# Performance work log

Hardware: AMD Instinct MI355X
Metric: run time of the kernel (lower is better)

The kernel has to match this reference:

```python
import jax, jax.numpy as jnp
import numpy as np

B, T, H = 32, 512, 1024

def setup_inputs() -> dict:
    key = jax.random.key(0)
    k1, k2, k3, k4, k5 = jax.random.split(key, 5)
    s = 1.0 / np.sqrt(H)  # torch LSTM init scale
    return {
        "x": jax.random.normal(k1, (B, T, H), dtype=jnp.float32),
        "w_ih": jax.random.uniform(k2, (4 * H, H), jnp.float32, -s, s),
        "w_hh": jax.random.uniform(k3, (4 * H, H), jnp.float32, -s, s),
        "b_ih": jax.random.uniform(k4, (4 * H,), jnp.float32, -s, s),
        "b_hh": jax.random.uniform(k5, (4 * H,), jnp.float32, -s, s),
    }

def reference(x, w_ih, w_hh, b_ih, b_hh):
    # Precompute input projections for all steps: [T, B, 4H]
    xg = jnp.einsum('bth,gh->tbg', x, w_ih) + b_ih + b_hh
    h0 = jnp.zeros((x.shape[0], H), x.dtype)
    c0 = jnp.zeros_like(h0)

    def step(carry, xg_t):
        h, c = carry
        gates = xg_t + h @ w_hh.T            # [B, 4H]
        i, f, g, o = jnp.split(gates, 4, axis=-1)  # torch order: i,f,g,o
        i = jax.nn.sigmoid(i)
        f = jax.nn.sigmoid(f)
        g = jnp.tanh(g)
        o = jax.nn.sigmoid(o)
        c = f * c + i * g
        h = o * jnp.tanh(c)
        return (h, c), None

    (h_n, _), _ = jax.lax.scan(step, (h0, c0), xg)
    return h_n  # [B, H] == h_n[0] in torch
```

## Files before the change

### kernel.cpp

```cpp
#include <hip/hip_runtime.h>
#include <cmath>

#define Tn 512
#define Bn 32
#define Hn 1024

typedef short bf16x8 __attribute__((ext_vector_type(8)));
typedef float f32x4 __attribute__((ext_vector_type(4)));

__device__ __forceinline__ unsigned short f2bf_rne(float f) {
    unsigned u = __float_as_uint(f);
    unsigned r = (u + 0x7fffu + ((u >> 16) & 1u)) >> 16;
    return (unsigned short)r;
}
__device__ __forceinline__ float bf2f(unsigned short h) {
    return __uint_as_float((unsigned)h << 16);
}
__device__ __forceinline__ bf16x8 cvt8(float4 a, float4 b) {
    union { unsigned u[4]; bf16x8 v; } o;
    o.u[0] = (unsigned)f2bf_rne(a.x) | ((unsigned)f2bf_rne(a.y) << 16);
    o.u[1] = (unsigned)f2bf_rne(a.z) | ((unsigned)f2bf_rne(a.w) << 16);
    o.u[2] = (unsigned)f2bf_rne(b.x) | ((unsigned)f2bf_rne(b.y) << 16);
    o.u[3] = (unsigned)f2bf_rne(b.z) | ((unsigned)f2bf_rne(b.w) << 16);
    return o.v;
}
__device__ __forceinline__ bf16x8 as_bf8(uint4 u) {
    union { uint4 q; bf16x8 v; } o; o.q = u; return o.v;
}

__device__ __forceinline__ void gstore_u32_sc(unsigned* p, unsigned v) {
    asm volatile("global_store_dword %0, %1, off sc0 sc1\n\t"
                 "s_waitcnt vmcnt(0)"
                 :: "v"(p), "v"(v) : "memory");
}
__device__ __forceinline__ uint4 gload_u4_sc(const unsigned* p) {
    uint4 r;
    asm volatile("global_load_dwordx4 %0, %1, off sc0 sc1\n\t"
                 "s_waitcnt vmcnt(0)"
                 : "=&v"(r) : "v"(p) : "memory");
    return r;
}
__device__ __forceinline__ void gload_h_sc(const unsigned short* b0,
                                           const unsigned short* b1,
                                           uint4* o0, uint4* o1) {
    asm volatile(
        "global_load_dwordx4 %0, %8, off sc0 sc1\n\t"
        "global_load_dwordx4 %1, %8, off offset:64 sc0 sc1\n\t"
        "global_load_dwordx4 %2, %8, off offset:128 sc0 sc1\n\t"
        "global_load_dwordx4 %3, %8, off offset:192 sc0 sc1\n\t"
        "global_load_dwordx4 %4, %9, off sc0 sc1\n\t"
        "global_load_dwordx4 %5, %9, off offset:64 sc0 sc1\n\t"
        "global_load_dwordx4 %6, %9, off offset:128 sc0 sc1\n\t"
        "global_load_dwordx4 %7, %9, off offset:192 sc0 sc1\n\t"
        "s_waitcnt vmcnt(0)"
        : "=&v"(o0[0]), "=&v"(o0[1]), "=&v"(o0[2]), "=&v"(o0[3]),
          "=&v"(o1[0]), "=&v"(o1[1]), "=&v"(o1[2]), "=&v"(o1[3])
        : "v"(b0), "v"(b1)
        : "memory");
}

__global__ void lstm_flags_init(unsigned* flags) { flags[threadIdx.x] = 0u; }

__global__ __launch_bounds__(512, 2) void lstm_persist_mfma(
    const float* __restrict__ x,
    const float* __restrict__ w_ih,
    const float* __restrict__ w_hh,
    const float* __restrict__ b_ih,
    const float* __restrict__ b_hh,
    unsigned short* __restrict__ hbuf,
    unsigned* __restrict__ flags,
    float* __restrict__ out)
{
    extern __shared__ char smem[];
    unsigned short* lds_w = (unsigned short*)smem;
    float* lds_r = (float*)(smem + 131584);
    float* lds_g = (float*)(smem + 131584 + 16384);

    const int tid = threadIdx.x;
    const int bj  = blockIdx.x;
    const int wv  = tid >> 6;
    const int ln  = tid & 63;
    const int l15 = ln & 15;
    const int qd  = ln >> 4;

    for (int i = 0; i < 16; ++i) {
        int slot = i * 512 + tid;
        int r    = slot >> 9;
        int f4   = slot & 511;
        int n    = (r >> 2) * Hn + bj * 4 + (r & 3);
        float4 v = (f4 < 256) ? ((const float4*)(w_ih + (size_t)n * Hn))[f4]
                              : ((const float4*)(w_hh + (size_t)n * Hn))[f4 - 256];
        unsigned short h0 = f2bf_rne(v.x), h1 = f2bf_rne(v.y);
        unsigned short h2 = f2bf_rne(v.z), h3 = f2bf_rne(v.w);
        unsigned short l0 = f2bf_rne(v.x - bf2f(h0)), l1 = f2bf_rne(v.y - bf2f(h1));
        unsigned short l2 = f2bf_rne(v.z - bf2f(h2)), l3 = f2bf_rne(v.w - bf2f(h3));
        uint2 ph, pl;
        ph.x = (unsigned)h0 | ((unsigned)h1 << 16);
        ph.y = (unsigned)h2 | ((unsigned)h3 << 16);
        pl.x = (unsigned)l0 | ((unsigned)l1 << 16);
        pl.y = (unsigned)l2 | ((unsigned)l3 << 16);
        *(uint2*)(lds_w + (size_t)r        * 2056 + f4 * 4) = ph;
        *(uint2*)(lds_w + (size_t)(r + 16) * 2056 + f4 * 4) = pl;
    }

    float bias0 = 0.f, bias1 = 0.f, bias2 = 0.f, bias3 = 0.f, creg = 0.f;
    if (tid < 128) {
        int col = bj * 4 + (tid & 3);
        bias0 = b_ih[col]          + b_hh[col];
        bias1 = b_ih[Hn + col]     + b_hh[Hn + col];
        bias2 = b_ih[2 * Hn + col] + b_hh[2 * Hn + col];
        bias3 = b_ih[3 * Hn + col] + b_hh[3 * Hn + col];
    }
    __syncthreads();

    const unsigned short* whi_base = lds_w + (size_t)l15 * 2056 + qd * 8;
    const unsigned short* wlo_base = lds_w + (size_t)(l15 + 16) * 2056 + qd * 8;
    const float* xr0 = x + (size_t)l15        * (Tn * Hn) + wv * 128 + qd * 8;
    const float* xr1 = x + (size_t)(16 + l15) * (Tn * Hn) + wv * 128 + qd * 8;
    const size_t hoff0 = (size_t)l15        * Hn + wv * 128 + qd * 8;
    const size_t hoff1 = (size_t)(16 + l15) * Hn + wv * 128 + qd * 8;

    float4 xa0[4], xb0[4], xa1[4], xb1[4];
    #pragma unroll
    for (int j = 0; j < 4; ++j) {
        xa0[j] = *(const float4*)(xr0 + j * 32);
        xb0[j] = *(const float4*)(xr0 + j * 32 + 4);
        xa1[j] = *(const float4*)(xr1 + j * 32);
        xb1[j] = *(const float4*)(xr1 + j * 32 + 4);
    }

    for (int t = 0; t < Tn; ++t) {
        f32x4 acc0 = {0.f, 0.f, 0.f, 0.f};
        f32x4 acc1 = {0.f, 0.f, 0.f, 0.f};

        float4 na0[4], nb0[4], na1[4], nb1[4];
        {
            const int tn = (t + 1 < Tn) ? (t + 1) : t;
            const float* p0 = xr0 + (size_t)tn * Hn;
            const float* p1 = xr1 + (size_t)tn * Hn;
            #pragma unroll
            for (int j = 0; j < 4; ++j) {
                na0[j] = *(const float4*)(p0 + j * 32);
                nb0[j] = *(const float4*)(p0 + j * 32 + 4);
                na1[j] = *(const float4*)(p1 + j * 32);
                nb1[j] = *(const float4*)(p1 + j * 32 + 4);
            }
        }

        #pragma unroll
        for (int j = 0; j < 4; ++j) {
            const int koff = wv * 128 + j * 32;
            bf16x8 ahi = *(const bf16x8*)(whi_base + koff);
            bf16x8 alo = *(const bf16x8*)(wlo_base + koff);
            bf16x8 bf0 = cvt8(xa0[j], xb0[j]);
            bf16x8 bf1 = cvt8(xa1[j], xb1[j]);
            acc0 = __builtin_amdgcn_mfma_f32_16x16x32_bf16(ahi, bf0, acc0, 0, 0, 0);
            acc0 = __builtin_amdgcn_mfma_f32_16x16x32_bf16(alo, bf0, acc0, 0, 0, 0);
            acc1 = __builtin_amdgcn_mfma_f32_16x16x32_bf16(ahi, bf1, acc1, 0, 0, 0);
            acc1 = __builtin_amdgcn_mfma_f32_16x16x32_bf16(alo, bf1, acc1, 0, 0, 0);
        }

        if (t > 0) {
            if (wv == 0) {
                const unsigned* fp = flags + ln * 4;
                for (;;) {
                    uint4 f = gload_u4_sc(fp);
                    unsigned mn = f.x < f.y ? f.x : f.y;
                    unsigned mo = f.z < f.w ? f.z : f.w;
                    mn = mn < mo ? mn : mo;
                    if (__all((int)(mn >= (unsigned)t))) break;
                }
            }
            __syncthreads();

            const unsigned short* hb = hbuf + (size_t)((t - 1) & 1) * (Bn * Hn);
            uint4 hf0[4], hf1[4];
            gload_h_sc(hb + hoff0, hb + hoff1, hf0, hf1);
            #pragma unroll
            for (int j = 0; j < 4; ++j) {
                const int koff = 1024 + wv * 128 + j * 32;
                bf16x8 ahi = *(const bf16x8*)(whi_base + koff);
                bf16x8 alo = *(const bf16x8*)(wlo_base + koff);
                bf16x8 bf0 = as_bf8(hf0[j]);
                bf16x8 bf1 = as_bf8(hf1[j]);
                acc0 = __builtin_amdgcn_mfma_f32_16x16x32_bf16(ahi, bf0, acc0, 0, 0, 0);
                acc0 = __builtin_amdgcn_mfma_f32_16x16x32_bf16(alo, bf0, acc0, 0, 0, 0);
                acc1 = __builtin_amdgcn_mfma_f32_16x16x32_bf16(ahi, bf1, acc1, 0, 0, 0);
                acc1 = __builtin_amdgcn_mfma_f32_16x16x32_bf16(alo, bf1, acc1, 0, 0, 0);
            }
        }

        {
            float* pr0 = lds_r + (wv * 2 + 0) * 256 + l15;
            float* pr1 = lds_r + (wv * 2 + 1) * 256 + l15;
            #pragma unroll
            for (int r = 0; r < 4; ++r) {
                pr0[(qd * 4 + r) * 16] = acc0[r];
                pr1[(qd * 4 + r) * 16] = acc1[r];
            }
        }
        __syncthreads();
        {
            const int np = tid >> 5, b = tid & 31;
            const int bt = b >> 4, c16 = b & 15;
            float s = 0.f;
            #pragma unroll
            for (int w8 = 0; w8 < 8; ++w8)
                s += lds_r[(w8 * 2 + bt) * 256 + np * 16 + c16];
            lds_g[np * 32 + b] = s;
        }
        __syncthreads();

        if (tid < 128) {
            const int b = tid >> 2, cl = tid & 3;
            float gi = lds_g[(0 * 4 + cl) * 32 + b] + bias0;
            float gf = lds_g[(1 * 4 + cl) * 32 + b] + bias1;
            float gg = lds_g[(2 * 4 + cl) * 32 + b] + bias2;
            float go = lds_g[(3 * 4 + cl) * 32 + b] + bias3;
            float iv = 1.f / (1.f + expf(-gi));
            float fv = 1.f / (1.f + expf(-gf));
            float gv = tanhf(gg);
            float ov = 1.f / (1.f + expf(-go));
            creg = fv * creg + iv * gv;
            float hn = ov * tanhf(creg);
            unsigned short hv = f2bf_rne(hn);
            unsigned up = (unsigned)__shfl_xor((int)(unsigned)hv, 1, 64);
            if (!(tid & 1)) {
                unsigned pack = (unsigned)hv | (up << 16);
                unsigned short* hw = hbuf + (size_t)(t & 1) * (Bn * Hn)
                                   + (size_t)b * Hn + bj * 4 + cl;
                gstore_u32_sc((unsigned*)hw, pack);
            }
            if (t == Tn - 1) out[(size_t)b * Hn + bj * 4 + cl] = hn;
        }
        __syncthreads();
        if (tid == 0)
            gstore_u32_sc(&flags[bj], (unsigned)(t + 1));

        #pragma unroll
        for (int j = 0; j < 4; ++j) {
            xa0[j] = na0[j]; xb0[j] = nb0[j];
            xa1[j] = na1[j]; xb1[j] = nb1[j];
        }
    }
}

extern "C" void kernel_launch(void* const* d_in, const int* in_sizes, int n_in,
                              void* d_out, int out_size, void* d_ws, size_t ws_size,
                              hipStream_t stream) {
    const float* x    = (const float*)d_in[0];
    const float* w_ih = (const float*)d_in[1];
    const float* w_hh = (const float*)d_in[2];
    const float* b_ih = (const float*)d_in[3];
    const float* b_hh = (const float*)d_in[4];
    float* out = (float*)d_out;

    char* ws = (char*)d_ws;
    unsigned*       flags = (unsigned*)ws;
    unsigned short* hbuf  = (unsigned short*)(ws + 1024);
    (void)in_sizes; (void)n_in; (void)out_size; (void)ws_size;

    const size_t smem_bytes = 131584 + 16384 + 2048;

    lstm_flags_init<<<dim3(1), dim3(256), 0, stream>>>(flags);
    lstm_persist_mfma<<<dim3(256), dim3(512), smem_bytes, stream>>>(
        x, w_ih, w_hh, b_ih, b_hh, hbuf, flags, out);
}
```

Before: 4.254 ms.

## Replace block barriers with per-wave flag polling and LDS counter release

Every wave now polls the per-block step flags itself instead of one wave polling followed by a block barrier. The gate reduction and activation step are merged into a single phase done by 16 lanes per wave, which removes one barrier and the lds_g buffer. The flag release now uses an LDS atomic counter, so the last wave to finish a step publishes the flag without a block-wide barrier. The change also splits hi and lo MFMA accumulators for more ILP, swaps in fast rcp/exp sigmoid and tanh, and drops the wait after the h store. The barrier-free ordering across lanes, waves and steps is subtle, and the flag is never written for the final step.

```diff
diff --git a/kernel.cpp b/kernel.cpp
--- a/kernel.cpp
+++ b/kernel.cpp
@@ -28,14 +28,25 @@
     union { uint4 q; bf16x8 v; } o; o.q = u; return o.v;
 }
 
+__device__ __forceinline__ float fsigf(float x) {
+    return __builtin_amdgcn_rcpf(1.f + __expf(-x));
+}
+__device__ __forceinline__ float ftanhf(float x) {
+    return 1.f - 2.f * __builtin_amdgcn_rcpf(1.f + __expf(2.f * x));
+}
+
 __device__ __forceinline__ void gstore_u32_sc(unsigned* p, unsigned v) {
     asm volatile("global_store_dword %0, %1, off sc0 sc1\n\t"
                  "s_waitcnt vmcnt(0)"
                  :: "v"(p), "v"(v) : "memory");
 }
-__device__ __forceinline__ uint4 gload_u4_sc(const unsigned* p) {
-    uint4 r;
-    asm volatile("global_load_dwordx4 %0, %1, off sc0 sc1\n\t"
+__device__ __forceinline__ void gstore_u32_nd(unsigned* p, unsigned v) {
+    asm volatile("global_store_dword %0, %1, off sc0 sc1"
+                 :: "v"(p), "v"(v) : "memory");
+}
+__device__ __forceinline__ unsigned gload_u32_sc(const unsigned* p) {
+    unsigned r;
+    asm volatile("global_load_dword %0, %1, off sc0 sc1\n\t"
                  "s_waitcnt vmcnt(0)"
                  : "=&v"(r) : "v"(p) : "memory");
     return r;
@@ -74,7 +85,7 @@
     extern __shared__ char smem[];
     unsigned short* lds_w = (unsigned short*)smem;
     float* lds_r = (float*)(smem + 131584);
-    float* lds_g = (float*)(smem + 131584 + 16384);
+    unsigned* lds_cnt = (unsigned*)(smem + 131584 + 16384);
 
     const int tid = threadIdx.x;
     const int bj  = blockIdx.x;
@@ -82,6 +93,8 @@
     const int ln  = tid & 63;
     const int l15 = ln & 15;
     const int qd  = ln >> 4;
+
+    if (tid == 0) *lds_cnt = 0u;
 
     for (int i = 0; i < 16; ++i) {
         int slot = i * 512 + tid;
@@ -104,8 +117,8 @@
     }
 
     float bias0 = 0.f, bias1 = 0.f, bias2 = 0.f, bias3 = 0.f, creg = 0.f;
-    if (tid < 128) {
-        int col = bj * 4 + (tid & 3);
+    if (ln < 16) {
+        int col = bj * 4 + (ln & 3);
         bias0 = b_ih[col]          + b_hh[col];
         bias1 = b_ih[Hn + col]     + b_hh[Hn + col];
         bias2 = b_ih[2 * Hn + col] + b_hh[2 * Hn + col];
@@ -130,8 +143,8 @@
     }
 
     for (int t = 0; t < Tn; ++t) {
-        f32x4 acc0 = {0.f, 0.f, 0.f, 0.f};
-        f32x4 acc1 = {0.f, 0.f, 0.f, 0.f};
+        f32x4 a0h = {0.f,0.f,0.f,0.f}, a0l = {0.f,0.f,0.f,0.f};
+        f32x4 a1h = {0.f,0.f,0.f,0.f}, a1l = {0.f,0.f,0.f,0.f};
 
         float4 na0[4], nb0[4], na1[4], nb1[4];
         {
@@ -154,25 +167,22 @@
             bf16x8 alo = *(const bf16x8*)(wlo_base + koff);
             bf16x8 bf0 = cvt8(xa0[j], xb0[j]);
             bf16x8 bf1 = cvt8(xa1[j], xb1[j]);
-            acc0 = __builtin_amdgcn_mfma_f32_16x16x32_bf16(ahi, bf0, acc0, 0, 0, 0);
-            acc0 = __builtin_amdgcn_mfma_f32_16x16x32_bf16(alo, bf0, acc0, 0, 0, 0);
-            acc1 = __builtin_amdgcn_mfma_f32_16x16x32_bf16(ahi, bf1, acc1, 0, 0, 0);
-            acc1 = __builtin_amdgcn_mfma_f32_16x16x32_bf16(alo, bf1, acc1, 0, 0, 0);
+            a0h = __builtin_amdgcn_mfma_f32_16x16x32_bf16(ahi, bf0, a0h, 0, 0, 0);
+            a0l = __builtin_amdgcn_mfma_f32_16x16x32_bf16(alo, bf0, a0l, 0, 0, 0);
+            a1h = __builtin_amdgcn_mfma_f32_16x16x32_bf16(ahi, bf1, a1h, 0, 0, 0);
+            a1l = __builtin_amdgcn_mfma_f32_16x16x32_bf16(alo, bf1, a1l, 0, 0, 0);
         }
 
         if (t > 0) {
-            if (wv == 0) {
-                const unsigned* fp = flags + ln * 4;
+            {
+                const int src = (ln < 32) ? (wv * 32 + ln) : bj;
+                const unsigned* fp = flags + src;
+                bool done = false;
                 for (;;) {
-                    uint4 f = gload_u4_sc(fp);
-                    unsigned mn = f.x < f.y ? f.x : f.y;
-                    unsigned mo = f.z < f.w ? f.z : f.w;
-                    mn = mn < mo ? mn : mo;
-                    if (__all((int)(mn >= (unsigned)t))) break;
+                    if (!done) done = (gload_u32_sc(fp) >= (unsigned)t);
+                    if (__all((int)done)) break;
                 }
             }
-            __syncthreads();
-
             const unsigned short* hb = hbuf + (size_t)((t - 1) & 1) * (Bn * Hn);
             uint4 hf0[4], hf1[4];
             gload_h_sc(hb + hoff0, hb + hoff1, hf0, hf1);
@@ -183,14 +193,16 @@
                 bf16x8 alo = *(const bf16x8*)(wlo_base + koff);
                 bf16x8 bf0 = as_bf8(hf0[j]);
                 bf16x8 bf1 = as_bf8(hf1[j]);
-                acc0 = __builtin_amdgcn_mfma_f32_16x16x32_bf16(ahi, bf0, acc0, 0, 0, 0);
-                acc0 = __builtin_amdgcn_mfma_f32_16x16x32_bf16(alo, bf0, acc0, 0, 0, 0);
-                acc1 = __builtin_amdgcn_mfma_f32_16x16x32_bf16(ahi, bf1, acc1, 0, 0, 0);
-                acc1 = __builtin_amdgcn_mfma_f32_16x16x32_bf16(alo, bf1, acc1, 0, 0, 0);
+                a0h = __builtin_amdgcn_mfma_f32_16x16x32_bf16(ahi, bf0, a0h, 0, 0, 0);
+                a0l = __builtin_amdgcn_mfma_f32_16x16x32_bf16(alo, bf0, a0l, 0, 0, 0);
+                a1h = __builtin_amdgcn_mfma_f32_16x16x32_bf16(ahi, bf1, a1h, 0, 0, 0);
+                a1l = __builtin_amdgcn_mfma_f32_16x16x32_bf16(alo, bf1, a1l, 0, 0, 0);
             }
         }
 
         {
+            f32x4 acc0 = a0h + a0l;
+            f32x4 acc1 = a1h + a1l;
             float* pr0 = lds_r + (wv * 2 + 0) * 256 + l15;
             float* pr1 = lds_r + (wv * 2 + 1) * 256 + l15;
             #pragma unroll
@@ -200,42 +212,43 @@
             }
         }
         __syncthreads();
-        {
-            const int np = tid >> 5, b = tid & 31;
-            const int bt = b >> 4, c16 = b & 15;
-            float s = 0.f;
-            #pragma unroll
-            for (int w8 = 0; w8 < 8; ++w8)
-                s += lds_r[(w8 * 2 + bt) * 256 + np * 16 + c16];
-            lds_g[np * 32 + b] = s;
-        }
-        __syncthreads();
-
-        if (tid < 128) {
-            const int b = tid >> 2, cl = tid & 3;
-            float gi = lds_g[(0 * 4 + cl) * 32 + b] + bias0;
-            float gf = lds_g[(1 * 4 + cl) * 32 + b] + bias1;
-            float gg = lds_g[(2 * 4 + cl) * 32 + b] + bias2;
-            float go = lds_g[(3 * 4 + cl) * 32 + b] + bias3;
-            float iv = 1.f / (1.f + expf(-gi));
-            float fv = 1.f / (1.f + expf(-gf));
-            float gv = tanhf(gg);
-            float ov = 1.f / (1.f + expf(-go));
+
+        if (ln < 16) {
+            const int e   = (wv << 4) | ln;
+            const int b   = e >> 2;
+            const int cl  = e & 3;
+            const int bt  = b >> 4, c16 = b & 15;
+            float s0 = 0.f, s1 = 0.f, s2 = 0.f, s3 = 0.f;
+            #pragma unroll
+            for (int w8 = 0; w8 < 8; ++w8) {
+                const float* base = lds_r + (w8 * 2 + bt) * 256 + c16;
+                s0 += base[(0 * 4 + cl) * 16];
+                s1 += base[(1 * 4 + cl) * 16];
+                s2 += base[(2 * 4 + cl) * 16];
+                s3 += base[(3 * 4 + cl) * 16];
+            }
+            float iv = fsigf(s0 + bias0);
+            float fv = fsigf(s1 + bias1);
+            float gv = ftanhf(s2 + bias2);
+            float ov = fsigf(s3 + bias3);
             creg = fv * creg + iv * gv;
-            float hn = ov * tanhf(creg);
+            float hn = ov * ftanhf(creg);
             unsigned short hv = f2bf_rne(hn);
             unsigned up = (unsigned)__shfl_xor((int)(unsigned)hv, 1, 64);
-            if (!(tid & 1)) {
+            if (!(ln & 1)) {
                 unsigned pack = (unsigned)hv | (up << 16);
                 unsigned short* hw = hbuf + (size_t)(t & 1) * (Bn * Hn)
                                    + (size_t)b * Hn + bj * 4 + cl;
-                gstore_u32_sc((unsigned*)hw, pack);
+                gstore_u32_nd((unsigned*)hw, pack);
             }
             if (t == Tn - 1) out[(size_t)b * Hn + bj * 4 + cl] = hn;
         }
-        __syncthreads();
-        if (tid == 0)
-            gstore_u32_sc(&flags[bj], (unsigned)(t + 1));
+        asm volatile("s_waitcnt vmcnt(0)" ::: "memory");
+        if (ln == 0) {
+            unsigned old = atomicAdd(lds_cnt, 1u);
+            if (old == 8u * (unsigned)t + 7u && (t + 1 < Tn))
+                gstore_u32_sc(&flags[bj], (unsigned)(t + 1));
+        }
 
         #pragma unroll
         for (int j = 0; j < 4; ++j) {
@@ -260,7 +273,7 @@
     unsigned short* hbuf  = (unsigned short*)(ws + 1024);
     (void)in_sizes; (void)n_in; (void)out_size; (void)ws_size;
 
-    const size_t smem_bytes = 131584 + 16384 + 2048;
+    const size_t smem_bytes = 131584 + 16384 + 16;
 
     lstm_flags_init<<<dim3(1), dim3(256), 0, stream>>>(flags);
     lstm_persist_mfma<<<dim3(256), dim3(512), smem_bytes, stream>>>(
```

After: 3.909 ms. 1.09x faster.
